# Kernel tuning notes

Measured on AMD Instinct MI355X. Metric: run time of the kernel, lower is better.

Reference implementation:

```python
import jax, jax.numpy as jnp
import numpy as np

N_NODES = 100000
N_EDGES = 1600000
D_IN = 128
D_OUT = 128


def setup_inputs() -> dict:
    key = jax.random.key(0)
    k1, k2, k3, k4, k5 = jax.random.split(key, 5)
    x = jax.random.normal(k1, (N_NODES, D_IN), dtype=jnp.float32)
    edge_index = jax.random.randint(k2, (2, N_EDGES), 0, N_NODES, dtype=jnp.int32)
    edge_weight = jax.random.uniform(k3, (N_EDGES,), dtype=jnp.float32)
    # xavier-uniform linear weight [out, in]
    limit = float(np.sqrt(6.0 / (D_IN + D_OUT)))
    W = jax.random.uniform(k4, (D_OUT, D_IN), dtype=jnp.float32, minval=-limit, maxval=limit)
    bias = jnp.zeros((D_OUT,), dtype=jnp.float32)
    prelu_a = jax.random.uniform(k5, (1,), dtype=jnp.float32)
    return {"x": x, "edge_index": edge_index, "edge_weight": edge_weight,
            "W": W, "bias": bias, "prelu_a": prelu_a}


def _prelu(x, a):
    return jnp.where(x >= 0, x, a * x)


def reference(x, edge_index, edge_weight, W, bias, prelu_a):
    # seq_fts = fc(x): [N, D_OUT]
    h = x @ W.T
    # sparse adjacency matmul: out[dst] += w_e * h[src]
    src, dst = edge_index[0], edge_index[1]
    msgs = h[src] * edge_weight[:, None]          # [E, D_OUT]
    agg = jax.ops.segment_sum(msgs, dst, num_segments=N_NODES)
    out = agg + bias                              # bias add
    out = _prelu(out, prelu_a)                    # GCN's PReLU
    return jax.nn.relu(out)                       # GCNGeneration.activation
```

## Files before the change

kernel.cpp:

```cpp
#include <hip/hip_runtime.h>

#define N_NODES 100000
#define N_EDGES 1600000
#define D 128

#define NCB   512
#define BR    196
#define CHUNK 8192
#define SLOTS 24
#define CAP   6144

#define XQ   (N_NODES * D / 4)
#define XQB  (XQ / 256)
#define WQ   (D * D / 4)
#define WQB  (WQ / 256)
#define HB   256

typedef __bf16 bf16x8 __attribute__((ext_vector_type(8)));
typedef float  f32x4  __attribute__((ext_vector_type(4)));
typedef unsigned short u16x8 __attribute__((ext_vector_type(8)));

static __device__ __forceinline__ unsigned short f2bf(float f) {
    union { float f; unsigned u; } v; v.f = f;
    unsigned r = v.u + 0x7FFFu + ((v.u >> 16) & 1u);
    return (unsigned short)(r >> 16);
}

static __device__ __forceinline__ void accum_row(
    float4& acc0, float4& acc1, const float4 u, const float wt)
{
    const unsigned qx = __float_as_uint(u.x);
    const unsigned qy = __float_as_uint(u.y);
    const unsigned qz = __float_as_uint(u.z);
    const unsigned qw = __float_as_uint(u.w);
    acc0.x += wt * __uint_as_float(qx << 16);
    acc0.y += wt * __uint_as_float(qx & 0xFFFF0000u);
    acc0.z += wt * __uint_as_float(qy << 16);
    acc0.w += wt * __uint_as_float(qy & 0xFFFF0000u);
    acc1.x += wt * __uint_as_float(qz << 16);
    acc1.y += wt * __uint_as_float(qz & 0xFFFF0000u);
    acc1.z += wt * __uint_as_float(qw << 16);
    acc1.w += wt * __uint_as_float(qw & 0xFFFF0000u);
}

__global__ __launch_bounds__(256) void k_prep(
    const float4* __restrict__ x4, ushort4* __restrict__ xh4,
    const float4* __restrict__ w4, ushort4* __restrict__ wh4,
    const int* __restrict__ ei, int* __restrict__ ghist)
{
    __shared__ int h[NCB];
    const int b = blockIdx.x;
    const int t = threadIdx.x;
    if (b < HB) {
        h[t] = 0; h[t + 256] = 0;
        __syncthreads();
        for (int e = b * 256 + t; e < N_EDGES; e += HB * 256)
            atomicAdd(&h[ei[N_EDGES + e] / BR], 1);
        __syncthreads();
        atomicAdd(&ghist[t], h[t]);
        atomicAdd(&ghist[t + 256], h[t + 256]);
    } else if (b < HB + XQB) {
        const int i = (b - HB) * 256 + t;
        const float4 v = x4[i];
        xh4[i] = make_ushort4(f2bf(v.x), f2bf(v.y), f2bf(v.z), f2bf(v.w));
    } else {
        const int i = (b - HB - XQB) * 256 + t;
        const float4 v = w4[i];
        wh4[i] = make_ushort4(f2bf(v.x), f2bf(v.y), f2bf(v.z), f2bf(v.w));
    }
}

__global__ __launch_bounds__(512) void k_cscan(
    const int* __restrict__ ghist, int* __restrict__ cOff, int* __restrict__ gcur)
{
    __shared__ int sh[NCB];
    const int t = threadIdx.x;
    const int v = ghist[t];
    sh[t] = v;
    __syncthreads();
    for (int d = 1; d < NCB; d <<= 1) {
        int u = (t >= d) ? sh[t - d] : 0;
        __syncthreads();
        sh[t] += u;
        __syncthreads();
    }
    const int excl = sh[t] - v;
    cOff[t] = excl;
    gcur[t] = excl;
    if (t == NCB - 1) cOff[NCB] = sh[NCB - 1];
}

__global__ __launch_bounds__(256, 1) void k_part(
    const int* __restrict__ ei, const float* __restrict__ ew,
    int* __restrict__ gcur, int2* __restrict__ part)
{
    __shared__ int2 bins[NCB * SLOTS];
    __shared__ int bcnt[NCB];
    __shared__ int bbase[NCB];
    const int t = threadIdx.x;
    const int e0 = blockIdx.x * CHUNK;

    bcnt[t] = 0; bcnt[t + 256] = 0;
    __syncthreads();

    #pragma unroll 8
    for (int k = 0; k < CHUNK / 256; ++k) {
        const int e = e0 + k * 256 + t;
        if (e < N_EDGES) {
            const int dst = ei[N_EDGES + e];
            const int src = ei[e];
            const int b = dst / BR;
            const int ld = dst - b * BR;
            const int2 p = make_int2(src | (ld << 17), __float_as_int(ew[e]));
            const int r = atomicAdd(&bcnt[b], 1);
            if (r < SLOTS) bins[b * SLOTS + r] = p;
            else {
                int pos = atomicAdd(&gcur[b], 1);
                part[pos] = p;
            }
        }
    }
    __syncthreads();

    {
        int c0 = min(bcnt[t], SLOTS);
        int c1 = min(bcnt[t + 256], SLOTS);
        bbase[t]       = c0 ? atomicAdd(&gcur[t], c0) : 0;
        bbase[t + 256] = c1 ? atomicAdd(&gcur[t + 256], c1) : 0;
        bcnt[t] = c0; bcnt[t + 256] = c1;
    }
    __syncthreads();

    for (int s = t; s < NCB * SLOTS; s += 256) {
        const int b = s / SLOTS;
        const int r = s - b * SLOTS;
        if (r < bcnt[b]) part[bbase[b] + r] = bins[s];
    }
}

__global__ __launch_bounds__(256) void k_csr(
    const int* __restrict__ cOff, int2* __restrict__ part, int* __restrict__ off)
{
    __shared__ int2 buf[CAP];
    __shared__ int nh[256];
    __shared__ int orig[256];
    __shared__ int cur[256];

    const int b = blockIdx.x;
    const int t = threadIdx.x;
    const int lo = b * BR;
    const int base = cOff[b];
    int cnt = cOff[b + 1] - base;
    if (cnt > CAP) cnt = CAP;

    nh[t] = 0;
    __syncthreads();

    for (int i = t; i < cnt; i += 256) {
        const int2 p = part[base + i];
        buf[i] = p;
        atomicAdd(&nh[((unsigned)p.x) >> 17], 1);
    }
    __syncthreads();
    orig[t] = nh[t];
    __syncthreads();
    for (int d = 1; d < 256; d <<= 1) {
        int u = (t >= d) ? nh[t - d] : 0;
        __syncthreads();
        nh[t] += u;
        __syncthreads();
    }
    const int excl = nh[t] - orig[t];
    cur[t] = excl;
    if (t < BR && lo + t < N_NODES) off[lo + t] = base + excl;
    if (b == NCB - 1 && t == 0) off[N_NODES] = cOff[NCB];
    __syncthreads();

    for (int i = t; i < cnt; i += 256) {
        const int2 p = buf[i];
        const int ld = ((unsigned)p.x) >> 17;
        const int r = atomicAdd(&cur[ld], 1);
        part[base + r] = make_int2(p.x & 0x1FFFF, p.y);
    }
}

__global__ __launch_bounds__(256) void k_gx(
    const float4* __restrict__ xh4,
    const int* __restrict__ off,
    const int2* __restrict__ pair,
    const unsigned short* __restrict__ wh,
    const float* __restrict__ bias, const float* __restrict__ pa,
    float* __restrict__ out)
{
    __shared__ unsigned short tb[16][136];

    const int tid = threadIdx.x;
    const int g   = tid >> 4;
    const int sl  = tid & 15;
    const int m0  = blockIdx.x << 4;
    const float aP = pa[0];

    {
        const int n = m0 + g;
        const int beg = off[n], end = off[n + 1];
        float4 acc0 = make_float4(0.f, 0.f, 0.f, 0.f);
        float4 acc1 = make_float4(0.f, 0.f, 0.f, 0.f);

        int e = beg;
        for (; e + 3 < end; e += 4) {
            const int2 p0 = pair[e + 0], p1 = pair[e + 1];
            const int2 p2 = pair[e + 2], p3 = pair[e + 3];
            const float4 u0 = xh4[p0.x * 16 + sl];
            const float4 u1 = xh4[p1.x * 16 + sl];
            const float4 u2 = xh4[p2.x * 16 + sl];
            const float4 u3 = xh4[p3.x * 16 + sl];
            accum_row(acc0, acc1, u0, __int_as_float(p0.y));
            accum_row(acc0, acc1, u1, __int_as_float(p1.y));
            accum_row(acc0, acc1, u2, __int_as_float(p2.y));
            accum_row(acc0, acc1, u3, __int_as_float(p3.y));
        }
        for (; e < end; ++e) {
            const int2 p = pair[e];
            const float4 u = xh4[p.x * 16 + sl];
            accum_row(acc0, acc1, u, __int_as_float(p.y));
        }

        u16x8 s;
        s[0] = f2bf(acc0.x); s[1] = f2bf(acc0.y);
        s[2] = f2bf(acc0.z); s[3] = f2bf(acc0.w);
        s[4] = f2bf(acc1.x); s[5] = f2bf(acc1.y);
        s[6] = f2bf(acc1.z); s[7] = f2bf(acc1.w);
        *(u16x8*)&tb[g][sl * 8] = s;
    }
    __syncthreads();

    const int lane = tid & 63;
    const int wv = tid >> 6;
    const int mm = lane & 15;
    const int quad = lane >> 4;

    bf16x8 af[4];
    #pragma unroll
    for (int c = 0; c < 4; ++c)
        af[c] = *(const bf16x8*)&tb[mm][c * 32 + quad * 8];

    #pragma unroll
    for (int t = 0; t < 2; ++t) {
        const int n = ((wv * 2 + t) << 4) + mm;
        f32x4 acc = {0.f, 0.f, 0.f, 0.f};
        #pragma unroll
        for (int c = 0; c < 4; ++c) {
            const bf16x8 bf = *(const bf16x8*)(wh + n * D + c * 32 + quad * 8);
            acc = __builtin_amdgcn_mfma_f32_16x16x32_bf16(af[c], bf, acc, 0, 0, 0);
        }
        const float bv = bias[n];
        #pragma unroll
        for (int r = 0; r < 4; ++r) {
            float v = acc[r] + bv;
            v = (v >= 0.f) ? v : aP * v;
            v = fmaxf(v, 0.f);
            out[(size_t)(m0 + (quad << 2) + r) * D + n] = v;
        }
    }
}

__global__ __launch_bounds__(256) void gcn_scatter(
    const float* __restrict__ x, const int* __restrict__ ei,
    const float* __restrict__ ew, float* __restrict__ agg)
{
    const int lane = threadIdx.x & 63;
    const int wave = (blockIdx.x * blockDim.x + threadIdx.x) >> 6;
    const int nwaves = (gridDim.x * blockDim.x) >> 6;
    for (int e = wave; e < N_EDGES; e += nwaves) {
        const int src = ei[e];
        const int dst = ei[N_EDGES + e];
        const float w = ew[e];
        const float2 v = ((const float2*)(x + (size_t)src * D))[lane];
        float* op = agg + (size_t)dst * D + lane * 2;
        unsafeAtomicAdd(op,     w * v.x);
        unsafeAtomicAdd(op + 1, w * v.y);
    }
}

#define MT 32
__global__ __launch_bounds__(256, 2) void gcn_transform(
    const float* __restrict__ A, const float* __restrict__ W,
    const float* __restrict__ bias, const float* __restrict__ pa,
    float* __restrict__ out)
{
    __shared__ float Wt[D][D];
    __shared__ float xs[MT][D];
    const int tid = threadIdx.x;
    const int row0 = blockIdx.x * MT;

    for (int j = tid; j < D * (D / 4); j += 256) {
        const int n = j & 127;
        const int kg = j >> 7;
        const float4 v = ((const float4*)W)[n * (D / 4) + kg];
        const int k4 = kg << 2;
        Wt[k4 + 0][n] = v.x; Wt[k4 + 1][n] = v.y;
        Wt[k4 + 2][n] = v.z; Wt[k4 + 3][n] = v.w;
    }
    for (int i = tid; i < MT * (D / 4); i += 256) {
        const int r = i >> 5;
        const int c4 = i & 31;
        ((float4*)xs[r])[c4] = ((const float4*)(A + (size_t)(row0 + r) * D))[c4];
    }
    __syncthreads();

    const int tn = tid & 31;
    const int tm = tid >> 5;
    float acc[4][4] = {};
    #pragma unroll
    for (int k = 0; k < D; k += 4) {
        const float4 wv0 = *(const float4*)&Wt[k + 0][tn * 4];
        const float4 wv1 = *(const float4*)&Wt[k + 1][tn * 4];
        const float4 wv2 = *(const float4*)&Wt[k + 2][tn * 4];
        const float4 wv3 = *(const float4*)&Wt[k + 3][tn * 4];
        #pragma unroll
        for (int i = 0; i < 4; ++i) {
            const float4 xv = *(const float4*)&xs[tm * 4 + i][k];
            acc[i][0] += xv.x * wv0.x + xv.y * wv1.x + xv.z * wv2.x + xv.w * wv3.x;
            acc[i][1] += xv.x * wv0.y + xv.y * wv1.y + xv.z * wv2.y + xv.w * wv3.y;
            acc[i][2] += xv.x * wv0.z + xv.y * wv1.z + xv.z * wv2.z + xv.w * wv3.z;
            acc[i][3] += xv.x * wv0.w + xv.y * wv1.w + xv.z * wv2.w + xv.w * wv3.w;
        }
    }
    const float a = pa[0];
    const float4 bv = ((const float4*)bias)[tn];
    #pragma unroll
    for (int i = 0; i < 4; ++i) {
        const int gr = row0 + tm * 4 + i;
        float t0 = acc[i][0] + bv.x, t1 = acc[i][1] + bv.y;
        float t2 = acc[i][2] + bv.z, t3 = acc[i][3] + bv.w;
        float4 r;
        r.x = fmaxf(t0 >= 0.f ? t0 : a * t0, 0.f);
        r.y = fmaxf(t1 >= 0.f ? t1 : a * t1, 0.f);
        r.z = fmaxf(t2 >= 0.f ? t2 : a * t2, 0.f);
        r.w = fmaxf(t3 >= 0.f ? t3 : a * t3, 0.f);
        ((float4*)(out + (size_t)gr * D))[tn] = r;
    }
}

extern "C" void kernel_launch(void* const* d_in, const int* in_sizes, int n_in,
                              void* d_out, int out_size, void* d_ws, size_t ws_size,
                              hipStream_t stream) {
    const float* x    = (const float*)d_in[0];
    const int*   ei   = (const int*)d_in[1];
    const float* ew   = (const float*)d_in[2];
    const float* W    = (const float*)d_in[3];
    const float* bias = (const float*)d_in[4];
    const float* pa   = (const float*)d_in[5];
    float* out = (float*)d_out;

    const size_t o_ghist = 0;
    const size_t o_cOff  = o_ghist + NCB;
    const size_t o_gcur  = o_cOff + NCB + 1;
    const size_t o_off   = o_gcur + NCB;
    const size_t o_part  = o_off + N_NODES + 1;
    const size_t o_wh    = (o_part + 2 * (size_t)N_EDGES + 3) & ~(size_t)3;
    const size_t o_xh    = o_wh + (size_t)D * D / 2;
    const size_t endA    = o_xh + (size_t)N_NODES * D / 2;
    const size_t needA   = endA * 4;

    int* wsb = (int*)d_ws;
    int* ghist = wsb + o_ghist;
    int* cOff  = wsb + o_cOff;
    int* gcur  = wsb + o_gcur;
    int* off   = wsb + o_off;
    int2* part = (int2*)(wsb + o_part);
    unsigned short* wh = (unsigned short*)(wsb + o_wh);
    unsigned short* xh = (unsigned short*)(wsb + o_xh);

    if (ws_size >= needA) {
        (void)hipMemsetAsync(ghist, 0, NCB * sizeof(int), stream);
        k_prep <<<HB + XQB + WQB, 256, 0, stream>>>(
            (const float4*)x, (ushort4*)xh, (const float4*)W, (ushort4*)wh, ei, ghist);
        k_cscan<<<1, NCB, 0, stream>>>(ghist, cOff, gcur);
        k_part <<<(N_EDGES + CHUNK - 1) / CHUNK, 256, 0, stream>>>(ei, ew, gcur, part);
        k_csr  <<<NCB, 256, 0, stream>>>(cOff, part, off);
        k_gx   <<<N_NODES / 16, 256, 0, stream>>>(
            (const float4*)xh, off, part, wh, bias, pa, out);
    } else {
        (void)hipMemsetAsync(out, 0, (size_t)N_NODES * D * sizeof(float), stream);
        gcn_scatter<<<12800, 256, 0, stream>>>(x, ei, ew, out);
        gcn_transform<<<N_NODES / MT, 256, 0, stream>>>(out, W, bias, pa, out);
    }
}
```

Measured before the change: 262.6 us.

## Fuse preprocessing kernels into one cooperative persistent kernel with grid syncs

Replaces the memset plus the prep, scan, partition and CSR-build kernels with a single cooperative kernel of 256 blocks that moves between phases using grid-wide syncs. Each block computes the bucket prefix scan redundantly in shared memory, so the separate scan kernel and cOff buffer go away. The bf16 conversion of x is split across two phases so it overlaps with the histogram and the scan. The aim is to remove launch gaps and inter-kernel drain. In exchange, parallelism is limited to one 256-thread block per CU, and four grid barriers are added.

```diff
diff --git a/kernel.cpp b/kernel.cpp
--- a/kernel.cpp
+++ b/kernel.cpp
@@ -1,4 +1,7 @@
 #include <hip/hip_runtime.h>
+#include <hip/hip_cooperative_groups.h>
+
+namespace cg = cooperative_groups;
 
 #define N_NODES 100000
 #define N_EDGES 1600000
@@ -6,15 +9,12 @@
 
 #define NCB   512
 #define BR    196
-#define CHUNK 8192
 #define SLOTS 24
 #define CAP   6144
+#define PB    256
 
 #define XQ   (N_NODES * D / 4)
-#define XQB  (XQ / 256)
 #define WQ   (D * D / 4)
-#define WQB  (WQ / 256)
-#define HB   256
 
 typedef __bf16 bf16x8 __attribute__((ext_vector_type(8)));
 typedef float  f32x4  __attribute__((ext_vector_type(4)));
@@ -43,144 +43,138 @@
     acc1.w += wt * __uint_as_float(qw & 0xFFFF0000u);
 }
 
-__global__ __launch_bounds__(256) void k_prep(
+__global__ __launch_bounds__(256, 1) void k_pre(
     const float4* __restrict__ x4, ushort4* __restrict__ xh4,
     const float4* __restrict__ w4, ushort4* __restrict__ wh4,
-    const int* __restrict__ ei, int* __restrict__ ghist)
-{
-    __shared__ int h[NCB];
+    const int* __restrict__ ei, const float* __restrict__ ew,
+    int* __restrict__ ghist, int* __restrict__ gcur,
+    int2* __restrict__ part, int* __restrict__ off)
+{
+    cg::grid_group grid = cg::this_grid();
+    __shared__ int2 bins[NCB * SLOTS];
+    __shared__ int coffl[NCB];
+    __shared__ int bcnt[NCB];
+    __shared__ int bbase[NCB];
+    __shared__ int sc[256];
+
     const int b = blockIdx.x;
     const int t = threadIdx.x;
-    if (b < HB) {
-        h[t] = 0; h[t + 256] = 0;
-        __syncthreads();
-        for (int e = b * 256 + t; e < N_EDGES; e += HB * 256)
-            atomicAdd(&h[ei[N_EDGES + e] / BR], 1);
-        __syncthreads();
-        atomicAdd(&ghist[t], h[t]);
-        atomicAdd(&ghist[t + 256], h[t + 256]);
-    } else if (b < HB + XQB) {
-        const int i = (b - HB) * 256 + t;
+    const int gt = b * 256 + t;
+
+    bcnt[t] = 0; bcnt[t + 256] = 0;
+    __syncthreads();
+    for (int e = gt; e < N_EDGES; e += PB * 256)
+        atomicAdd(&bcnt[ei[N_EDGES + e] / BR], 1);
+    if (b == 0) { ghist[t] = 0; ghist[t + 256] = 0; }
+    if (b == 1) {
+        for (int i = t; i < WQ; i += 256) {
+            const float4 v = w4[i];
+            wh4[i] = make_ushort4(f2bf(v.x), f2bf(v.y), f2bf(v.z), f2bf(v.w));
+        }
+    }
+    for (int i = gt; i < XQ / 2; i += PB * 256) {
         const float4 v = x4[i];
         xh4[i] = make_ushort4(f2bf(v.x), f2bf(v.y), f2bf(v.z), f2bf(v.w));
-    } else {
-        const int i = (b - HB - XQB) * 256 + t;
-        const float4 v = w4[i];
-        wh4[i] = make_ushort4(f2bf(v.x), f2bf(v.y), f2bf(v.z), f2bf(v.w));
-    }
-}
-
-__global__ __launch_bounds__(512) void k_cscan(
-    const int* __restrict__ ghist, int* __restrict__ cOff, int* __restrict__ gcur)
-{
-    __shared__ int sh[NCB];
-    const int t = threadIdx.x;
-    const int v = ghist[t];
-    sh[t] = v;
-    __syncthreads();
-    for (int d = 1; d < NCB; d <<= 1) {
-        int u = (t >= d) ? sh[t - d] : 0;
-        __syncthreads();
-        sh[t] += u;
-        __syncthreads();
-    }
-    const int excl = sh[t] - v;
-    cOff[t] = excl;
-    gcur[t] = excl;
-    if (t == NCB - 1) cOff[NCB] = sh[NCB - 1];
-}
-
-__global__ __launch_bounds__(256, 1) void k_part(
-    const int* __restrict__ ei, const float* __restrict__ ew,
-    int* __restrict__ gcur, int2* __restrict__ part)
-{
-    __shared__ int2 bins[NCB * SLOTS];
-    __shared__ int bcnt[NCB];
-    __shared__ int bbase[NCB];
-    const int t = threadIdx.x;
-    const int e0 = blockIdx.x * CHUNK;
+    }
+    grid.sync();
+
+    atomicAdd(&ghist[t], bcnt[t]);
+    atomicAdd(&ghist[t + 256], bcnt[t + 256]);
+    for (int i = XQ / 2 + gt; i < XQ; i += PB * 256) {
+        const float4 v = x4[i];
+        xh4[i] = make_ushort4(f2bf(v.x), f2bf(v.y), f2bf(v.z), f2bf(v.w));
+    }
+    grid.sync();
+
+    {
+        const int a0 = ghist[2 * t], a1 = ghist[2 * t + 1];
+        const int ps = a0 + a1;
+        sc[t] = ps;
+        __syncthreads();
+        for (int d = 1; d < 256; d <<= 1) {
+            const int u = (t >= d) ? sc[t - d] : 0;
+            __syncthreads();
+            sc[t] += u;
+            __syncthreads();
+        }
+        const int ex = sc[t] - ps;
+        coffl[2 * t]     = ex;
+        coffl[2 * t + 1] = ex + a0;
+        if (b == 0) { gcur[2 * t] = ex; gcur[2 * t + 1] = ex + a0; }
+    }
+    grid.sync();
 
     bcnt[t] = 0; bcnt[t + 256] = 0;
     __syncthreads();
-
-    #pragma unroll 8
-    for (int k = 0; k < CHUNK / 256; ++k) {
-        const int e = e0 + k * 256 + t;
-        if (e < N_EDGES) {
+    {
+        const int e0 = b * (N_EDGES / PB);
+        const int e1 = e0 + (N_EDGES / PB);
+        for (int e = e0 + t; e < e1; e += 256) {
             const int dst = ei[N_EDGES + e];
             const int src = ei[e];
-            const int b = dst / BR;
-            const int ld = dst - b * BR;
+            const int bk = dst / BR;
+            const int ld = dst - bk * BR;
             const int2 p = make_int2(src | (ld << 17), __float_as_int(ew[e]));
-            const int r = atomicAdd(&bcnt[b], 1);
-            if (r < SLOTS) bins[b * SLOTS + r] = p;
-            else {
-                int pos = atomicAdd(&gcur[b], 1);
-                part[pos] = p;
-            }
-        }
-    }
-    __syncthreads();
-
+            const int r = atomicAdd(&bcnt[bk], 1);
+            if (r < SLOTS) bins[bk * SLOTS + r] = p;
+            else part[atomicAdd(&gcur[bk], 1)] = p;
+        }
+    }
+    __syncthreads();
     {
-        int c0 = min(bcnt[t], SLOTS);
-        int c1 = min(bcnt[t + 256], SLOTS);
+        const int c0 = min(bcnt[t], SLOTS);
+        const int c1 = min(bcnt[t + 256], SLOTS);
         bbase[t]       = c0 ? atomicAdd(&gcur[t], c0) : 0;
         bbase[t + 256] = c1 ? atomicAdd(&gcur[t + 256], c1) : 0;
         bcnt[t] = c0; bcnt[t + 256] = c1;
     }
     __syncthreads();
-
     for (int s = t; s < NCB * SLOTS; s += 256) {
-        const int b = s / SLOTS;
-        const int r = s - b * SLOTS;
-        if (r < bcnt[b]) part[bbase[b] + r] = bins[s];
-    }
-}
-
-__global__ __launch_bounds__(256) void k_csr(
-    const int* __restrict__ cOff, int2* __restrict__ part, int* __restrict__ off)
-{
-    __shared__ int2 buf[CAP];
-    __shared__ int nh[256];
-    __shared__ int orig[256];
-    __shared__ int cur[256];
-
-    const int b = blockIdx.x;
-    const int t = threadIdx.x;
-    const int lo = b * BR;
-    const int base = cOff[b];
-    int cnt = cOff[b + 1] - base;
-    if (cnt > CAP) cnt = CAP;
-
-    nh[t] = 0;
-    __syncthreads();
-
-    for (int i = t; i < cnt; i += 256) {
-        const int2 p = part[base + i];
-        buf[i] = p;
-        atomicAdd(&nh[((unsigned)p.x) >> 17], 1);
-    }
-    __syncthreads();
-    orig[t] = nh[t];
-    __syncthreads();
-    for (int d = 1; d < 256; d <<= 1) {
-        int u = (t >= d) ? nh[t - d] : 0;
-        __syncthreads();
-        nh[t] += u;
-        __syncthreads();
-    }
-    const int excl = nh[t] - orig[t];
-    cur[t] = excl;
-    if (t < BR && lo + t < N_NODES) off[lo + t] = base + excl;
-    if (b == NCB - 1 && t == 0) off[N_NODES] = cOff[NCB];
-    __syncthreads();
-
-    for (int i = t; i < cnt; i += 256) {
-        const int2 p = buf[i];
-        const int ld = ((unsigned)p.x) >> 17;
-        const int r = atomicAdd(&cur[ld], 1);
-        part[base + r] = make_int2(p.x & 0x1FFFF, p.y);
+        const int bk = s / SLOTS;
+        const int r = s - bk * SLOTS;
+        if (r < bcnt[bk]) part[bbase[bk] + r] = bins[s];
+    }
+    grid.sync();
+
+    int2* buf = bins;
+    int* nh = bcnt;
+    int* orig = bbase;
+    int* cur = sc;
+    for (int half = 0; half < 2; ++half) {
+        const int bk = 2 * b + half;
+        const int base = coffl[bk];
+        const int tot = (bk == NCB - 1) ? N_EDGES : coffl[bk + 1];
+        int cnt = tot - base;
+        if (cnt > CAP) cnt = CAP;
+        __syncthreads();
+        nh[t] = 0;
+        __syncthreads();
+        for (int i = t; i < cnt; i += 256) {
+            const int2 p = part[base + i];
+            buf[i] = p;
+            atomicAdd(&nh[((unsigned)p.x) >> 17], 1);
+        }
+        __syncthreads();
+        orig[t] = nh[t];
+        __syncthreads();
+        for (int d = 1; d < 256; d <<= 1) {
+            const int u = (t >= d) ? nh[t - d] : 0;
+            __syncthreads();
+            nh[t] += u;
+            __syncthreads();
+        }
+        const int excl = nh[t] - orig[t];
+        cur[t] = excl;
+        const int lo = bk * BR;
+        if (t < BR && lo + t < N_NODES) off[lo + t] = base + excl;
+        if (bk == NCB - 1 && t == 0) off[N_NODES] = N_EDGES;
+        __syncthreads();
+        for (int i = t; i < cnt; i += 256) {
+            const int2 p = buf[i];
+            const int ld = ((unsigned)p.x) >> 17;
+            const int r = atomicAdd(&cur[ld], 1);
+            part[base + r] = make_int2(p.x & 0x1FFFF, p.y);
+        }
     }
 }
 
@@ -354,10 +348,9 @@
     float* out = (float*)d_out;
 
     const size_t o_ghist = 0;
-    const size_t o_cOff  = o_ghist + NCB;
-    const size_t o_gcur  = o_cOff + NCB + 1;
-    const size_t o_off   = o_gcur + NCB;
-    const size_t o_part  = o_off + N_NODES + 1;
+    const size_t o_gcur  = 512;
+    const size_t o_off   = 1024;
+    const size_t o_part  = 101026;
     const size_t o_wh    = (o_part + 2 * (size_t)N_EDGES + 3) & ~(size_t)3;
     const size_t o_xh    = o_wh + (size_t)D * D / 2;
     const size_t endA    = o_xh + (size_t)N_NODES * D / 2;
@@ -365,7 +358,6 @@
 
     int* wsb = (int*)d_ws;
     int* ghist = wsb + o_ghist;
-    int* cOff  = wsb + o_cOff;
     int* gcur  = wsb + o_gcur;
     int* off   = wsb + o_off;
     int2* part = (int2*)(wsb + o_part);
@@ -373,13 +365,21 @@
     unsigned short* xh = (unsigned short*)(wsb + o_xh);
 
     if (ws_size >= needA) {
-        (void)hipMemsetAsync(ghist, 0, NCB * sizeof(int), stream);
-        k_prep <<<HB + XQB + WQB, 256, 0, stream>>>(
-            (const float4*)x, (ushort4*)xh, (const float4*)W, (ushort4*)wh, ei, ghist);
-        k_cscan<<<1, NCB, 0, stream>>>(ghist, cOff, gcur);
-        k_part <<<(N_EDGES + CHUNK - 1) / CHUNK, 256, 0, stream>>>(ei, ew, gcur, part);
-        k_csr  <<<NCB, 256, 0, stream>>>(cOff, part, off);
-        k_gx   <<<N_NODES / 16, 256, 0, stream>>>(
+        const float4* x4p = (const float4*)x;
+        ushort4* xh4p = (ushort4*)xh;
+        const float4* w4p = (const float4*)W;
+        ushort4* wh4p = (ushort4*)wh;
+        const int* eip = ei;
+        const float* ewp = ew;
+        int* ghistp = ghist;
+        int* gcurp = gcur;
+        int2* partp = part;
+        int* offp = off;
+        void* ka[] = { &x4p, &xh4p, &w4p, &wh4p, &eip, &ewp,
+                       &ghistp, &gcurp, &partp, &offp };
+        (void)hipLaunchCooperativeKernel((void*)k_pre, dim3(PB), dim3(256),
+                                         ka, 0u, stream);
+        k_gx<<<N_NODES / 16, 256, 0, stream>>>(
             (const float4*)xh, off, part, wh, bias, pa, out);
     } else {
         (void)hipMemsetAsync(out, 0, (size_t)N_NODES * D * sizeof(float), stream);
```

Measured after the change: 400.1 us. +52.4%, slower.
